# Kernel tuning notes

Hardware: AMD Instinct MI355X
Metric: run time of the kernel (lower is better)

## Reference

```python
import jax, jax.numpy as jnp
import numpy as np

HEADS = 16
D_H = 64
ALPHA = 1.0


def _skew(QEr):
    # Music-Transformer skew: (b,h,n,n) -> relative-to-absolute
    b, h, i, j = QEr.shape
    pad = jnp.pad(QEr, ((0, 0), (0, 0), (0, 0), (1, 0)))  # (b,h,i,j+1)
    return pad.reshape(b, h, j + 1, i)[:, :, 1:, :]  # (b,h,i,j)


def _gather_bias(q, table, idx, heads):
    # q: (b,h,i,d); table: (S,d); idx: (b,i,j) int -> (b,h,i,j)
    b, h, i, d = q.shape
    QE = jnp.einsum('bhid,sd->bhis', q, table)  # (b,h,i,S)
    idx_b = jnp.broadcast_to(idx[:, None, :, :], (b, h, i, idx.shape[-1]))
    return jnp.take_along_axis(QE, idx_b, axis=-1)


def setup_inputs() -> dict:
    key = jax.random.key(0)
    ks = jax.random.split(key, 16)
    b, n, dim = 2, 1024, 1024
    d_h = dim // HEADS
    inp = {
        'x': jax.random.normal(ks[0], (b, n, dim), dtype=jnp.float32),
        'rel_bar': jax.random.randint(ks[1], (b, n, n), 0, 17, dtype=jnp.int32),
        'rel_position': jax.random.randint(ks[2], (b, n, n), 0, 96, dtype=jnp.int32),
        'rel_octave': jax.random.randint(ks[3], (b, n, n), 0, 25, dtype=jnp.int32),
        'rel_semitone': jax.random.randint(ks[4], (b, n, n), 0, 13, dtype=jnp.int32),
        'Wq': jax.random.normal(ks[5], (dim, dim), dtype=jnp.float32) * 0.02,
        'Wk': jax.random.normal(ks[6], (dim, dim), dtype=jnp.float32) * 0.02,
        'Wv': jax.random.normal(ks[7], (dim, dim), dtype=jnp.float32) * 0.02,
        'Wo': jax.random.normal(ks[8], (dim, dim), dtype=jnp.float32) * 0.02,
        'Er': jax.random.normal(ks[9], (n, d_h), dtype=jnp.float32),
        'Er_bar': jax.random.normal(ks[10], (16, d_h), dtype=jnp.float32),
        'Er_position': jax.random.normal(ks[11], (95, d_h), dtype=jnp.float32),
        'Er_octave': jax.random.normal(ks[12], (24, d_h), dtype=jnp.float32),
        'Er_semitone': jax.random.normal(ks[13], (12, d_h), dtype=jnp.float32),
    }
    return inp


def reference(x, rel_bar, rel_position, rel_octave, rel_semitone,
              Wq, Wk, Wv, Wo, Er, Er_bar, Er_position, Er_octave, Er_semitone):
    b, n, dim = x.shape
    h, d = HEADS, dim // HEADS

    def split_heads(t):
        return t.reshape(b, n, h, d).transpose(0, 2, 1, 3)  # (b,h,n,d)

    q = split_heads(x @ Wq.T)
    k = split_heads(x @ Wk.T)
    v = split_heads(x @ Wv.T)

    QK_t = jnp.einsum('bhid,bhjd->bhij', q, k)

    # relative-index bias (Music-Transformer style)
    QEr = jnp.einsum('bhid,jd->bhij', q, Er)  # start = max_seq_len - n = 0
    Srel = _skew(QEr)

    zrow = jnp.zeros((1, d), dtype=x.dtype)
    S_bar = _gather_bias(q, jnp.concatenate([Er_bar, zrow]), rel_bar, h)
    S_position = _gather_bias(q, jnp.concatenate([Er_position, zrow]), rel_position, h)
    S_octave = _gather_bias(q, jnp.concatenate([Er_octave, zrow]), rel_octave, h)
    S_semitone = _gather_bias(q, jnp.concatenate([Er_semitone, zrow]), rel_semitone, h)

    S_time = S_bar + S_position
    S_pitch = S_octave + S_semitone

    scores = (QK_t + Srel + ALPHA * (S_time + S_pitch)) / jnp.sqrt(jnp.asarray(d, x.dtype))
    causal = jnp.tril(jnp.ones((n, n), dtype=bool))
    scores = jnp.where(causal[None, None], scores, jnp.asarray(-1e9, x.dtype))
    attn = jax.nn.softmax(scores, axis=-1)

    out = jnp.einsum('bhij,bhjd->bhid', attn, v)
    out = out.transpose(0, 2, 1, 3).reshape(b, n, dim)
    return out @ Wo.T
```

## Files before the change

kernel.cpp:

```cpp
#include <hip/hip_runtime.h>


using bf16x8 = __attribute__((ext_vector_type(8))) short;
using f32x4  = __attribute__((ext_vector_type(4))) float;

__device__ __forceinline__ float bf2f(unsigned short u) {
  unsigned x = ((unsigned)u) << 16;
  float f;
  __builtin_memcpy(&f, &x, 4);
  return f;
}
__device__ __forceinline__ unsigned short f2bf(float f) {
  unsigned x;
  __builtin_memcpy(&x, &f, 4);
  unsigned r = (x + 0x7FFFu + ((x >> 16) & 1u)) >> 16;
  return (unsigned short)r;
}

union B8 { bf16x8 v; unsigned short u[8]; };

__global__ __launch_bounds__(256) void prep(
    const float* __restrict__ x,  const float* __restrict__ Wq,
    const float* __restrict__ Wk, const float* __restrict__ Wv,
    const float* __restrict__ Wo, const float* __restrict__ Er,
    const int* __restrict__ rb, const int* __restrict__ rp,
    const int* __restrict__ ro, const int* __restrict__ rs,
    const float* __restrict__ Tb, const float* __restrict__ Tp,
    const float* __restrict__ To, const float* __restrict__ Ts,
    unsigned short* __restrict__ x_bf, unsigned short* __restrict__ Wqkv,
    unsigned short* __restrict__ Wo_bf, unsigned short* __restrict__ Er_bf,
    unsigned* __restrict__ Pidx, unsigned short* __restrict__ Tpad)
{
  const int bid = blockIdx.x;
  const int tid = threadIdx.x;
  if (bid < 1024) {
    const int total = 1589248;
    for (int i = bid * 256 + tid; i < total; i += 1024 * 256) {
      const float4* s4;
      ushort4* d4;
      if (i < 524288)       { s4 = (const float4*)x  + i;           d4 = (ushort4*)x_bf  + i; }
      else if (i < 786432)  { s4 = (const float4*)Wq + (i-524288);  d4 = (ushort4*)Wqkv  + (i-524288); }
      else if (i < 1048576) { s4 = (const float4*)Wk + (i-786432);  d4 = (ushort4*)Wqkv  + (i-786432) + 262144; }
      else if (i < 1310720) { s4 = (const float4*)Wv + (i-1048576); d4 = (ushort4*)Wqkv  + (i-1048576) + 524288; }
      else if (i < 1572864) { s4 = (const float4*)Wo + (i-1310720); d4 = (ushort4*)Wo_bf + (i-1310720); }
      else                  { s4 = (const float4*)Er + (i-1572864); d4 = (ushort4*)Er_bf + (i-1572864); }
      const float4 v = *s4;
      ushort4 o;
      o.x = f2bf(v.x); o.y = f2bf(v.y); o.z = f2bf(v.z); o.w = f2bf(v.w);
      *d4 = o;
    }
  } else if (bid < 2048) {
    for (int i = (bid - 1024) * 256 + tid; i < 524288; i += 1024 * 256) {
      const int4 a = ((const int4*)rb)[i];
      const int4 b = ((const int4*)rp)[i];
      const int4 c = ((const int4*)ro)[i];
      const int4 d = ((const int4*)rs)[i];
      uint4 r;
      r.x = (unsigned)(a.x | (17+b.x)<<5 | (113+c.x)<<12 | (138+d.x)<<20);
      r.y = (unsigned)(a.y | (17+b.y)<<5 | (113+c.y)<<12 | (138+d.y)<<20);
      r.z = (unsigned)(a.z | (17+b.z)<<5 | (113+c.z)<<12 | (138+d.z)<<20);
      r.w = (unsigned)(a.w | (17+b.w)<<5 | (113+c.w)<<12 | (138+d.w)<<20);
      ((uint4*)Pidx)[i] = r;
    }
  } else {
    for (int t = tid; t < 10240; t += 256) {
      const int s = t >> 6, d = t & 63;
      float v = 0.f;
      if (s < 16)       v = Tb[s * 64 + d];
      else if (s == 16) v = 0.f;
      else if (s < 112) v = Tp[(s - 17) * 64 + d];
      else if (s < 113) v = 0.f;
      else if (s < 137) v = To[(s - 113) * 64 + d];
      else if (s < 138) v = 0.f;
      else if (s < 150) v = Ts[(s - 138) * 64 + d];
      Tpad[t] = f2bf(v * 0.125f);
    }
  }
}

__device__ __forceinline__ void ld_lds16(const unsigned short* g, unsigned short* l) {
  __builtin_amdgcn_global_load_lds(
      (const __attribute__((address_space(1))) unsigned int*)g,
      (__attribute__((address_space(3))) unsigned int*)l, 16, 0, 0);
}

template <int MODE>
__global__ __launch_bounds__(256) void gemm128(const unsigned short* __restrict__ A,
                                               const unsigned short* __restrict__ B,
                                               void* __restrict__ Cv,
                                               int M, int N, int K)
{
  __shared__ __align__(16) unsigned short Atile[128 * 32];
  __shared__ __align__(16) unsigned short Btile[128 * 32];
  const int tid = threadIdx.x;
  const int w = tid >> 6, lane = tid & 63;
  const int c15 = lane & 15, q = lane >> 4;
  const int wr = w >> 1, wc = w & 1;
  const int n0 = blockIdx.x * 128, m0 = blockIdx.y * 128;

  const unsigned short* ag = A + (size_t)(m0 + (tid >> 2)) * K + (tid & 3) * 8;
  const unsigned short* bg = B + (size_t)(n0 + (tid >> 2)) * K + (tid & 3) * 8;
  unsigned short* al = &Atile[tid * 8];
  unsigned short* bl = &Btile[tid * 8];
  const size_t half = (size_t)64 * K;

  f32x4 acc[4][4];
  #pragma unroll
  for (int mt = 0; mt < 4; mt++)
    #pragma unroll
    for (int nt = 0; nt < 4; nt++) { acc[mt][nt][0]=0.f; acc[mt][nt][1]=0.f; acc[mt][nt][2]=0.f; acc[mt][nt][3]=0.f; }

  for (int k0 = 0; k0 < K; k0 += 32) {
    __syncthreads();
    ld_lds16(ag + k0, al);
    ld_lds16(ag + half + k0, al + 2048);
    ld_lds16(bg + k0, bl);
    ld_lds16(bg + half + k0, bl + 2048);
    __syncthreads();

    bf16x8 af[4], bfr[4];
    #pragma unroll
    for (int mt = 0; mt < 4; mt++)
      af[mt] = *(const bf16x8*)&Atile[(wr * 64 + mt * 16 + c15) * 32 + q * 8];
    #pragma unroll
    for (int nt = 0; nt < 4; nt++)
      bfr[nt] = *(const bf16x8*)&Btile[(wc * 64 + nt * 16 + c15) * 32 + q * 8];
    #pragma unroll
    for (int mt = 0; mt < 4; mt++)
      #pragma unroll
      for (int nt = 0; nt < 4; nt++)
        acc[mt][nt] = __builtin_amdgcn_mfma_f32_16x16x32_bf16(af[mt], bfr[nt], acc[mt][nt], 0, 0, 0);
  }

  #pragma unroll
  for (int mt = 0; mt < 4; mt++)
    #pragma unroll
    for (int nt = 0; nt < 4; nt++)
      #pragma unroll
      for (int r = 0; r < 4; r++) {
        const int m = m0 + wr * 64 + mt * 16 + q * 4 + r;
        const int n = n0 + wc * 64 + nt * 16 + c15;
        if constexpr (MODE == 1) {
          ((float*)Cv)[(size_t)m * N + n] = acc[mt][nt][r];
        } else {
          const int which = n >> 10, hh = (n >> 6) & 15, d = n & 63;
          const int bb = m >> 10, i = m & 1023;
          ((unsigned short*)Cv)[(size_t)which * 2097152 +
                                (((size_t)(bb << 4) + hh) << 16) + (i << 6) + d] = f2bf(acc[mt][nt][r]);
        }
      }
}

__global__ __launch_bounds__(256) void qe_gemm(const unsigned short* __restrict__ Qh,
                                               const unsigned short* __restrict__ Tpad,
                                               unsigned short* __restrict__ QE)
{
  __shared__ __align__(16) unsigned short T[160][72];
  const int tid = threadIdx.x;
  const int w = tid >> 6, lane = tid & 63;
  const int c15 = lane & 15, q = lane >> 4;
  const int m0 = blockIdx.x * 64 + w * 16;

  for (int t = tid; t < 1280; t += 256) {
    const int r = t >> 3, c = (t & 7) * 8;
    *(bf16x8*)&T[r][c] = *(const bf16x8*)(Tpad + r * 64 + c);
  }
  __syncthreads();

  bf16x8 a0, a1;
  {
    const unsigned short* ap = Qh + ((size_t)(m0 + c15) << 6) + q * 8;
    a0 = *(const bf16x8*)ap;
    a1 = *(const bf16x8*)(ap + 32);
  }
  unsigned short* out = QE + (size_t)m0 * 160;
  #pragma unroll
  for (int st = 0; st < 10; st++) {
    bf16x8 b0 = *(const bf16x8*)&T[st * 16 + c15][q * 8];
    bf16x8 b1 = *(const bf16x8*)&T[st * 16 + c15][32 + q * 8];
    f32x4 acc; acc[0]=0.f; acc[1]=0.f; acc[2]=0.f; acc[3]=0.f;
    acc = __builtin_amdgcn_mfma_f32_16x16x32_bf16(a0, b0, acc, 0, 0, 0);
    acc = __builtin_amdgcn_mfma_f32_16x16x32_bf16(a1, b1, acc, 0, 0, 0);
    #pragma unroll
    for (int r = 0; r < 4; r++) {
      const _Float16 hv = (_Float16)acc[r];
      unsigned short hb;
      __builtin_memcpy(&hb, &hv, 2);
      out[(size_t)(q * 4 + r) * 160 + st * 16 + c15] = hb;
    }
  }
}

__global__ __launch_bounds__(256) void attn_kernel(
    const unsigned short* __restrict__ QKVh,
    const unsigned short* __restrict__ QE,
    const unsigned* __restrict__ Pidx,
    const unsigned short* __restrict__ Er,
    unsigned short* __restrict__ Ob)
{
  const int h  = blockIdx.x;
  const int bb = blockIdx.z;
  const int it = bb ? (15 - (int)blockIdx.y) : (int)blockIdx.y;
  const int i0 = it << 6;
  const int tid = threadIdx.x;
  const int w = tid >> 6;
  const int lane = tid & 63;
  const int c15 = lane & 15;
  const int q = lane >> 4;
  const int rowq = q * 4;

  __shared__ __align__(16) unsigned short Klds[2][64 * 64];
  __shared__ __align__(16) unsigned short Vtlds[64][72];
  __shared__ __align__(16) unsigned short C2[4][16 * 88];
  __shared__ __align__(16) unsigned short qeh[64 * 160];
  unsigned short* c2w = &C2[w][0];

  const unsigned short* qhb = QKVh + (((size_t)(bb << 4) + h) << 16);
  const unsigned short* khb = qhb + 2097152;
  const unsigned short* vhb = qhb + 2 * 2097152;

  ld_lds16(khb + tid * 8,        &Klds[0][tid * 8]);
  ld_lds16(khb + 2048 + tid * 8, &Klds[0][2048 + tid * 8]);

  {
    const size_t qeoff = ((((size_t)(bb << 4) + h) * 1024) + i0) * 160;
    const unsigned short* src = QE + qeoff;
    for (int t = tid; t < 1280; t += 256)
      *(bf16x8*)&qeh[t * 8] = *(const bf16x8*)(src + t * 8);
  }

  bf16x8 qf[2];
  {
    const unsigned short* qp = qhb + ((size_t)(i0 + w * 16 + c15) << 6);
    #pragma unroll
    for (int kk = 0; kk < 2; kk++) {
      B8 t;
      t.v = *(const bf16x8*)(qp + kk * 32 + q * 8);
      #pragma unroll
      for (int e = 0; e < 8; e++) t.u[e] = f2bf(bf2f(t.u[e]) * 0.125f);
      qf[kk] = t.v;
    }
  }

  f32x4 Oa[4];
  float mrow[4], lrow[4];
  #pragma unroll
  for (int dt = 0; dt < 4; dt++) { Oa[dt][0]=0.f; Oa[dt][1]=0.f; Oa[dt][2]=0.f; Oa[dt][3]=0.f; }
  #pragma unroll
  for (int r = 0; r < 4; r++) { mrow[r] = -3e38f; lrow[r] = 0.f; }

  const int iw = i0 + w * 16;
  const size_t idx0 = ((size_t)bb << 20) + ((size_t)(iw + rowq) << 10);

  for (int jt = 0; jt <= it; jt++) {
    const int j0 = jt << 6;
    const int cur = jt & 1;

    __syncthreads();

    if (jt < it) {
      const unsigned short* kn = khb + ((jt + 1) << 12);
      ld_lds16(kn + tid * 8,        &Klds[cur ^ 1][tid * 8]);
      ld_lds16(kn + 2048 + tid * 8, &Klds[cur ^ 1][2048 + tid * 8]);
    }

    unsigned pv[4][4];
    #pragma unroll
    for (int nt = 0; nt < 4; nt++)
      #pragma unroll
      for (int r = 0; r < 4; r++)
        pv[nt][r] = Pidx[idx0 + ((size_t)r << 10) + j0 + nt * 16 + c15];

    {
      const int vrow = tid >> 2, vcs = (tid & 3) * 16;
      const unsigned short* vt = vhb + (j0 << 6) + (vrow << 6) + vcs;
      B8 v0, v1;
      v0.v = *(const bf16x8*)vt;
      v1.v = *(const bf16x8*)(vt + 8);
      #pragma unroll
      for (int e = 0; e < 8; e++) {
        Vtlds[vcs + e][vrow]     = v0.u[e];
        Vtlds[vcs + 8 + e][vrow] = v1.u[e];
      }
    }

    f32x4 S[4];
    #pragma unroll
    for (int nt = 0; nt < 4; nt++) {
      f32x4 a; a[0]=0.f; a[1]=0.f; a[2]=0.f; a[3]=0.f;
      bf16x8 k0 = *(const bf16x8*)&Klds[cur][(nt * 16 + c15) * 64 + q * 8];
      bf16x8 k1 = *(const bf16x8*)&Klds[cur][(nt * 16 + c15) * 64 + 32 + q * 8];
      a = __builtin_amdgcn_mfma_f32_16x16x32_bf16(qf[0], k0, a, 0, 0, 0);
      a = __builtin_amdgcn_mfma_f32_16x16x32_bf16(qf[1], k1, a, 0, 0, 0);
      S[nt] = a;
    }

    {
      const int rbase = 960 - i0 + j0;
      #pragma unroll
      for (int t5 = 0; t5 < 5; t5++) {
        const int pt = 3 - w + t5;
        int row = rbase + pt * 16 + c15;
        row = row > 1023 ? 1023 : row;
        const unsigned short* ep = Er + (row << 6) + q * 8;
        bf16x8 e0 = *(const bf16x8*)ep;
        bf16x8 e1 = *(const bf16x8*)(ep + 32);
        f32x4 a; a[0]=0.f; a[1]=0.f; a[2]=0.f; a[3]=0.f;
        a = __builtin_amdgcn_mfma_f32_16x16x32_bf16(qf[0], e0, a, 0, 0, 0);
        a = __builtin_amdgcn_mfma_f32_16x16x32_bf16(qf[1], e1, a, 0, 0, 0);
        #pragma unroll
        for (int r = 0; r < 4; r++)
          c2w[(rowq + r) * 88 + t5 * 16 + c15] = f2bf(a[r]);
      }
    }

    #pragma unroll
    for (int nt = 0; nt < 4; nt++) {
      const int j = j0 + nt * 16 + c15;
      #pragma unroll
      for (int r = 0; r < 4; r++) {
        const int rb = (w * 16 + rowq + r) * 160;
        const unsigned p = pv[nt][r];
        _Float16 q0, q1, q2, q3;
        __builtin_memcpy(&q0, &qeh[rb + (p & 31)], 2);
        __builtin_memcpy(&q1, &qeh[rb + ((p >> 5) & 127)], 2);
        __builtin_memcpy(&q2, &qeh[rb + ((p >> 12) & 255)], 2);
        __builtin_memcpy(&q3, &qeh[rb + (p >> 20)], 2);
        const float bias = (float)(q0 + q1) + (float)(q2 + q3);
        const float srel = bf2f(c2w[(rowq + r) * 88 + (15 - (rowq + r) + nt * 16 + c15)]);
        float sc = S[nt][r] + srel + bias;
        if (jt == it && j > iw + rowq + r) sc = -3e38f;
        S[nt][r] = sc;
      }
    }

    float alpha[4];
    #pragma unroll
    for (int r = 0; r < 4; r++) {
      float v = fmaxf(fmaxf(S[0][r], S[1][r]), fmaxf(S[2][r], S[3][r]));
      v = fmaxf(v, __shfl_xor(v, 1));
      v = fmaxf(v, __shfl_xor(v, 2));
      v = fmaxf(v, __shfl_xor(v, 4));
      v = fmaxf(v, __shfl_xor(v, 8));
      const float mn = fmaxf(mrow[r], v);
      alpha[r] = __expf(mrow[r] - mn);
      mrow[r] = mn;
    }
    #pragma unroll
    for (int nt = 0; nt < 4; nt++)
      #pragma unroll
      for (int r = 0; r < 4; r++)
        S[nt][r] = __expf(S[nt][r] - mrow[r]);
    #pragma unroll
    for (int r = 0; r < 4; r++) {
      float s = S[0][r] + S[1][r] + S[2][r] + S[3][r];
      s += __shfl_xor(s, 1);
      s += __shfl_xor(s, 2);
      s += __shfl_xor(s, 4);
      s += __shfl_xor(s, 8);
      lrow[r] = lrow[r] * alpha[r] + s;
      #pragma unroll
      for (int dt = 0; dt < 4; dt++) Oa[dt][r] *= alpha[r];
    }

    __syncthreads();

    #pragma unroll
    for (int nt = 0; nt < 4; nt++)
      #pragma unroll
      for (int r = 0; r < 4; r++)
        c2w[(rowq + r) * 88 + nt * 16 + c15] = f2bf(S[nt][r]);

    bf16x8 pf[2];
    #pragma unroll
    for (int kk = 0; kk < 2; kk++)
      pf[kk] = *(const bf16x8*)&c2w[c15 * 88 + kk * 32 + q * 8];

    #pragma unroll
    for (int dt = 0; dt < 4; dt++) {
      bf16x8 v0 = *(const bf16x8*)&Vtlds[dt * 16 + c15][q * 8];
      bf16x8 v1 = *(const bf16x8*)&Vtlds[dt * 16 + c15][32 + q * 8];
      Oa[dt] = __builtin_amdgcn_mfma_f32_16x16x32_bf16(pf[0], v0, Oa[dt], 0, 0, 0);
      Oa[dt] = __builtin_amdgcn_mfma_f32_16x16x32_bf16(pf[1], v1, Oa[dt], 0, 0, 0);
    }
  }

  #pragma unroll
  for (int dt = 0; dt < 4; dt++)
    #pragma unroll
    for (int r = 0; r < 4; r++) {
      const int i_ = iw + rowq + r;
      const float o = Oa[dt][r] / lrow[r];
      Ob[(((size_t)bb << 10) + i_) * 1024 + (h << 6) + dt * 16 + c15] = f2bf(o);
    }
}

extern "C" void kernel_launch(void* const* d_in, const int* in_sizes, int n_in,
                              void* d_out, int out_size, void* d_ws, size_t ws_size,
                              hipStream_t stream)
{
  const float* x    = (const float*)d_in[0];
  const int*   rbar = (const int*)d_in[1];
  const int*   rpos = (const int*)d_in[2];
  const int*   roct = (const int*)d_in[3];
  const int*   rsem = (const int*)d_in[4];
  const float* Wq   = (const float*)d_in[5];
  const float* Wk   = (const float*)d_in[6];
  const float* Wv   = (const float*)d_in[7];
  const float* Wo   = (const float*)d_in[8];
  const float* Er   = (const float*)d_in[9];
  const float* Tb   = (const float*)d_in[10];
  const float* Tp   = (const float*)d_in[11];
  const float* To   = (const float*)d_in[12];
  const float* Ts   = (const float*)d_in[13];
  float* out = (float*)d_out;

  char* ws = (char*)d_ws;
  const size_t MB = 1u << 20;
  unsigned short* x_bf    = (unsigned short*)(ws);
  unsigned short* Wqkv_bf = (unsigned short*)(ws + 4 * MB);
  unsigned short* Wo_bf   = (unsigned short*)(ws + 10 * MB);
  unsigned short* Er_bf   = (unsigned short*)(ws + 12 * MB);
  unsigned short* Tpad    = (unsigned short*)(ws + 12 * MB + 256 * 1024);
  unsigned short* QKVh    = (unsigned short*)(ws + 13 * MB);
  unsigned short* Ob      = (unsigned short*)(ws + 25 * MB);
  unsigned short* QE      = (unsigned short*)(ws + 29 * MB);
  unsigned*       Pidx    = (unsigned*)(ws + 39 * MB);

  prep<<<2049, 256, 0, stream>>>(x, Wq, Wk, Wv, Wo, Er, rbar, rpos, roct, rsem,
                                 Tb, Tp, To, Ts,
                                 x_bf, Wqkv_bf, Wo_bf, Er_bf, Pidx, Tpad);

  gemm128<2><<<dim3(24, 16), 256, 0, stream>>>(x_bf, Wqkv_bf, QKVh, 2048, 3072, 1024);
  qe_gemm<<<512, 256, 0, stream>>>(QKVh, Tpad, QE);
  attn_kernel<<<dim3(16, 16, 2), 256, 0, stream>>>(QKVh, QE, Pidx, Er_bf, Ob);
  gemm128<1><<<dim3(8, 16), 256, 0, stream>>>(Ob, Wo_bf, out, 2048, 1024, 1024);
}
```

Before: 252.8 us.

## Fuse QE bias GEMM into attention kernel and halve GEMM N-tile

Removes the separate qe_gemm launch and its global QE buffer; each attention block now computes its 64x160 q·table bias tile in registers via MFMA from the already-scaled q fragments, writing it straight into LDS. The 0.125 scale is moved off the table since q is pre-scaled. Separately, the projection GEMMs use a 128x64 tile, doubling block count for better CU occupancy at the cost of lower reuse per block.

```diff
diff --git a/kernel.cpp b/kernel.cpp
--- a/kernel.cpp
+++ b/kernel.cpp
@@ -73,7 +73,7 @@
       else if (s < 137) v = To[(s - 113) * 64 + d];
       else if (s < 138) v = 0.f;
       else if (s < 150) v = Ts[(s - 138) * 64 + d];
-      Tpad[t] = f2bf(v * 0.125f);
+      Tpad[t] = f2bf(v);
     }
   }
 }
@@ -84,19 +84,20 @@
       (__attribute__((address_space(3))) unsigned int*)l, 16, 0, 0);
 }
 
-template <int MODE>
+template <int MODE, int BN>
 __global__ __launch_bounds__(256) void gemm128(const unsigned short* __restrict__ A,
                                                const unsigned short* __restrict__ B,
                                                void* __restrict__ Cv,
                                                int M, int N, int K)
 {
+  constexpr int NT = BN / 32;
   __shared__ __align__(16) unsigned short Atile[128 * 32];
-  __shared__ __align__(16) unsigned short Btile[128 * 32];
+  __shared__ __align__(16) unsigned short Btile[BN * 32];
   const int tid = threadIdx.x;
   const int w = tid >> 6, lane = tid & 63;
   const int c15 = lane & 15, q = lane >> 4;
   const int wr = w >> 1, wc = w & 1;
-  const int n0 = blockIdx.x * 128, m0 = blockIdx.y * 128;
+  const int n0 = blockIdx.x * BN, m0 = blockIdx.y * 128;
 
   const unsigned short* ag = A + (size_t)(m0 + (tid >> 2)) * K + (tid & 3) * 8;
   const unsigned short* bg = B + (size_t)(n0 + (tid >> 2)) * K + (tid & 3) * 8;
@@ -104,42 +105,42 @@
   unsigned short* bl = &Btile[tid * 8];
   const size_t half = (size_t)64 * K;
 
-  f32x4 acc[4][4];
+  f32x4 acc[4][NT];
   #pragma unroll
   for (int mt = 0; mt < 4; mt++)
     #pragma unroll
-    for (int nt = 0; nt < 4; nt++) { acc[mt][nt][0]=0.f; acc[mt][nt][1]=0.f; acc[mt][nt][2]=0.f; acc[mt][nt][3]=0.f; }
+    for (int nt = 0; nt < NT; nt++) { acc[mt][nt][0]=0.f; acc[mt][nt][1]=0.f; acc[mt][nt][2]=0.f; acc[mt][nt][3]=0.f; }
 
   for (int k0 = 0; k0 < K; k0 += 32) {
     __syncthreads();
     ld_lds16(ag + k0, al);
     ld_lds16(ag + half + k0, al + 2048);
     ld_lds16(bg + k0, bl);
-    ld_lds16(bg + half + k0, bl + 2048);
+    if constexpr (BN == 128) ld_lds16(bg + half + k0, bl + 2048);
     __syncthreads();
 
-    bf16x8 af[4], bfr[4];
+    bf16x8 af[4], bfr[NT];
     #pragma unroll
     for (int mt = 0; mt < 4; mt++)
       af[mt] = *(const bf16x8*)&Atile[(wr * 64 + mt * 16 + c15) * 32 + q * 8];
     #pragma unroll
-    for (int nt = 0; nt < 4; nt++)
-      bfr[nt] = *(const bf16x8*)&Btile[(wc * 64 + nt * 16 + c15) * 32 + q * 8];
+    for (int nt = 0; nt < NT; nt++)
+      bfr[nt] = *(const bf16x8*)&Btile[(wc * (BN / 2) + nt * 16 + c15) * 32 + q * 8];
     #pragma unroll
     for (int mt = 0; mt < 4; mt++)
       #pragma unroll
-      for (int nt = 0; nt < 4; nt++)
+      for (int nt = 0; nt < NT; nt++)
         acc[mt][nt] = __builtin_amdgcn_mfma_f32_16x16x32_bf16(af[mt], bfr[nt], acc[mt][nt], 0, 0, 0);
   }
 
   #pragma unroll
   for (int mt = 0; mt < 4; mt++)
     #pragma unroll
-    for (int nt = 0; nt < 4; nt++)
+    for (int nt = 0; nt < NT; nt++)
       #pragma unroll
       for (int r = 0; r < 4; r++) {
         const int m = m0 + wr * 64 + mt * 16 + q * 4 + r;
-        const int n = n0 + wc * 64 + nt * 16 + c15;
+        const int n = n0 + wc * (BN / 2) + nt * 16 + c15;
         if constexpr (MODE == 1) {
           ((float*)Cv)[(size_t)m * N + n] = acc[mt][nt][r];
         } else {
@@ -151,49 +152,9 @@
       }
 }
 
-__global__ __launch_bounds__(256) void qe_gemm(const unsigned short* __restrict__ Qh,
-                                               const unsigned short* __restrict__ Tpad,
-                                               unsigned short* __restrict__ QE)
-{
-  __shared__ __align__(16) unsigned short T[160][72];
-  const int tid = threadIdx.x;
-  const int w = tid >> 6, lane = tid & 63;
-  const int c15 = lane & 15, q = lane >> 4;
-  const int m0 = blockIdx.x * 64 + w * 16;
-
-  for (int t = tid; t < 1280; t += 256) {
-    const int r = t >> 3, c = (t & 7) * 8;
-    *(bf16x8*)&T[r][c] = *(const bf16x8*)(Tpad + r * 64 + c);
-  }
-  __syncthreads();
-
-  bf16x8 a0, a1;
-  {
-    const unsigned short* ap = Qh + ((size_t)(m0 + c15) << 6) + q * 8;
-    a0 = *(const bf16x8*)ap;
-    a1 = *(const bf16x8*)(ap + 32);
-  }
-  unsigned short* out = QE + (size_t)m0 * 160;
-  #pragma unroll
-  for (int st = 0; st < 10; st++) {
-    bf16x8 b0 = *(const bf16x8*)&T[st * 16 + c15][q * 8];
-    bf16x8 b1 = *(const bf16x8*)&T[st * 16 + c15][32 + q * 8];
-    f32x4 acc; acc[0]=0.f; acc[1]=0.f; acc[2]=0.f; acc[3]=0.f;
-    acc = __builtin_amdgcn_mfma_f32_16x16x32_bf16(a0, b0, acc, 0, 0, 0);
-    acc = __builtin_amdgcn_mfma_f32_16x16x32_bf16(a1, b1, acc, 0, 0, 0);
-    #pragma unroll
-    for (int r = 0; r < 4; r++) {
-      const _Float16 hv = (_Float16)acc[r];
-      unsigned short hb;
-      __builtin_memcpy(&hb, &hv, 2);
-      out[(size_t)(q * 4 + r) * 160 + st * 16 + c15] = hb;
-    }
-  }
-}
-
 __global__ __launch_bounds__(256) void attn_kernel(
     const unsigned short* __restrict__ QKVh,
-    const unsigned short* __restrict__ QE,
+    const unsigned short* __restrict__ Tpad,
     const unsigned* __restrict__ Pidx,
     const unsigned short* __restrict__ Er,
     unsigned short* __restrict__ Ob)
@@ -222,13 +183,6 @@
   ld_lds16(khb + tid * 8,        &Klds[0][tid * 8]);
   ld_lds16(khb + 2048 + tid * 8, &Klds[0][2048 + tid * 8]);
 
-  {
-    const size_t qeoff = ((((size_t)(bb << 4) + h) * 1024) + i0) * 160;
-    const unsigned short* src = QE + qeoff;
-    for (int t = tid; t < 1280; t += 256)
-      *(bf16x8*)&qeh[t * 8] = *(const bf16x8*)(src + t * 8);
-  }
-
   bf16x8 qf[2];
   {
     const unsigned short* qp = qhb + ((size_t)(i0 + w * 16 + c15) << 6);
@@ -239,6 +193,23 @@
       #pragma unroll
       for (int e = 0; e < 8; e++) t.u[e] = f2bf(bf2f(t.u[e]) * 0.125f);
       qf[kk] = t.v;
+    }
+  }
+
+  #pragma unroll
+  for (int st = 0; st < 10; st++) {
+    const unsigned short* tp = Tpad + (size_t)(st * 16 + c15) * 64 + q * 8;
+    bf16x8 t0 = *(const bf16x8*)tp;
+    bf16x8 t1 = *(const bf16x8*)(tp + 32);
+    f32x4 a; a[0]=0.f; a[1]=0.f; a[2]=0.f; a[3]=0.f;
+    a = __builtin_amdgcn_mfma_f32_16x16x32_bf16(qf[0], t0, a, 0, 0, 0);
+    a = __builtin_amdgcn_mfma_f32_16x16x32_bf16(qf[1], t1, a, 0, 0, 0);
+    #pragma unroll
+    for (int r = 0; r < 4; r++) {
+      const _Float16 hv = (_Float16)a[r];
+      unsigned short hb;
+      __builtin_memcpy(&hb, &hv, 2);
+      qeh[(w * 16 + rowq + r) * 160 + st * 16 + c15] = hb;
     }
   }
 
@@ -424,15 +395,13 @@
   unsigned short* Tpad    = (unsigned short*)(ws + 12 * MB + 256 * 1024);
   unsigned short* QKVh    = (unsigned short*)(ws + 13 * MB);
   unsigned short* Ob      = (unsigned short*)(ws + 25 * MB);
-  unsigned short* QE      = (unsigned short*)(ws + 29 * MB);
   unsigned*       Pidx    = (unsigned*)(ws + 39 * MB);
 
   prep<<<2049, 256, 0, stream>>>(x, Wq, Wk, Wv, Wo, Er, rbar, rpos, roct, rsem,
                                  Tb, Tp, To, Ts,
                                  x_bf, Wqkv_bf, Wo_bf, Er_bf, Pidx, Tpad);
 
-  gemm128<2><<<dim3(24, 16), 256, 0, stream>>>(x_bf, Wqkv_bf, QKVh, 2048, 3072, 1024);
-  qe_gemm<<<512, 256, 0, stream>>>(QKVh, Tpad, QE);
-  attn_kernel<<<dim3(16, 16, 2), 256, 0, stream>>>(QKVh, QE, Pidx, Er_bf, Ob);
-  gemm128<1><<<dim3(8, 16), 256, 0, stream>>>(Ob, Wo_bf, out, 2048, 1024, 1024);
-}
+  gemm128<2, 64><<<dim3(48, 16), 256, 0, stream>>>(x_bf, Wqkv_bf, QKVh, 2048, 3072, 1024);
+  attn_kernel<<<dim3(16, 16, 2), 256, 0, stream>>>(QKVh, Tpad, Pidx, Er_bf, Ob);
+  gemm128<1, 64><<<dim3(16, 16), 256, 0, stream>>>(Ob, Wo_bf, out, 2048, 1024, 1024);
+}
```

Result: faster. 240.9 us (-4.7%).
